# Kernel optimization log

Hardware: AMD Instinct MI355X
Metric: run time of the kernel (lower is better)

Reference implementation:

```python
import jax, jax.numpy as jnp
import numpy as np

B, S, H, NH = 2, 2048, 1024, 16
DH = H // NH
FF = 4 * H
EPS = 1e-5


def setup_inputs() -> dict:
    key = jax.random.key(0)
    ks = jax.random.split(key, 16)
    sd = 0.02
    inp = {
        "x": jax.random.normal(ks[0], (B, S, H), dtype=jnp.float32),
        "Wq": jax.random.normal(ks[1], (H, H), dtype=jnp.float32) * sd,
        "bq": jnp.zeros((H,), jnp.float32),
        "Wk": jax.random.normal(ks[2], (H, H), dtype=jnp.float32) * sd,
        "bk": jnp.zeros((H,), jnp.float32),
        "Wv": jax.random.normal(ks[3], (H, H), dtype=jnp.float32) * sd,
        "bv": jnp.zeros((H,), jnp.float32),
        "Wo": jax.random.normal(ks[4], (H, H), dtype=jnp.float32) * sd,
        "bo": jnp.zeros((H,), jnp.float32),
        "W1": jax.random.normal(ks[5], (H, FF), dtype=jnp.float32) * sd,
        "b1": jnp.zeros((FF,), jnp.float32),
        "W2": jax.random.normal(ks[6], (FF, H), dtype=jnp.float32) * sd,
        "b2": jnp.zeros((H,), jnp.float32),
        "g1": jnp.ones((H,), jnp.float32),
        "be1": jnp.zeros((H,), jnp.float32),
        "g2": jnp.ones((H,), jnp.float32),
        "be2": jnp.zeros((H,), jnp.float32),
    }
    return inp


def _layernorm(x, g, b):
    mu = jnp.mean(x, axis=-1, keepdims=True)
    var = jnp.mean(jnp.square(x - mu), axis=-1, keepdims=True)
    return (x - mu) * jax.lax.rsqrt(var + EPS) * g + b


def _block(x, Wq, bq, Wk, bk, Wv, bv, Wo, bo, W1, b1, W2, b2, g1, be1, g2, be2):
    # pre-LN attention
    h = _layernorm(x, g1, be1)
    q = (h @ Wq + bq).reshape(B, S, NH, DH)
    k = (h @ Wk + bk).reshape(B, S, NH, DH)
    v = (h @ Wv + bv).reshape(B, S, NH, DH)
    scale = DH ** -0.5
    scores = jnp.einsum("bqhd,bkhd->bhqk", q, k) * scale  # [B,NH,S,S]
    causal = jnp.tril(jnp.ones((S, S), dtype=bool))
    scores = jnp.where(causal, scores, -jnp.inf)
    attn = jax.nn.softmax(scores, axis=-1)
    out = jnp.einsum("bhqk,bkhd->bqhd", attn, v).reshape(B, S, H)
    x = x + (out @ Wo + bo)
    # pre-LN FFN with exact GELU (torch nn.GELU default)
    h = _layernorm(x, g2, be2)
    h = jax.nn.gelu(h @ W1 + b1, approximate=False)
    return x + (h @ W2 + b2)


def reference(x, Wq, bq, Wk, bk, Wv, bv, Wo, bo, W1, b1, W2, b2, g1, be1, g2, be2):
    return _block(x, Wq, bq, Wk, bk, Wv, bv, Wo, bo, W1, b1, W2, b2, g1, be1, g2, be2)
```

## Files before the change

### kernel.cpp

```cpp
#include <hip/hip_runtime.h>
#include <cstdint>
#include <cstddef>

typedef unsigned short u16;
typedef __attribute__((ext_vector_type(8))) __bf16 bf16v8;
typedef __attribute__((ext_vector_type(8))) unsigned short u16x8;
typedef __attribute__((ext_vector_type(4))) float f32x4;

constexpr int Bc = 2, Sc = 2048, Hc = 1024, NHc = 16, DHc = 64, FFc = 4096;
constexpr int Mc = Bc * Sc;

__device__ __forceinline__ u16 f2bf(float f) {
  unsigned u = __builtin_bit_cast(unsigned, f);
  return (u16)((u + 0x7FFFu + ((u >> 16) & 1u)) >> 16);
}

__device__ __forceinline__ int xcd_swz(int bid, int n) {
  const int q = n >> 3;
  return (bid & 7) * q + (bid >> 3);
}

__device__ __forceinline__ void gload_lds16(const void* g, void* l) {
  __builtin_amdgcn_global_load_lds(
      (const __attribute__((address_space(1))) unsigned*)(uintptr_t)g,
      (__attribute__((address_space(3))) unsigned*)(unsigned)(uintptr_t)l,
      16, 0, 0);
}

struct WP4 { const float* w0; const float* w1; const float* w2; const float* w3; };
__global__ __launch_bounds__(256) void wconv4_kernel(WP4 p, u16* __restrict__ Wt) {
  __shared__ float tile[64][65];
  const float* W = (blockIdx.z == 0) ? p.w0 : (blockIdx.z == 1) ? p.w1
                  : (blockIdx.z == 2) ? p.w2 : p.w3;
  u16* dst = Wt + (size_t)blockIdx.z * 1024 * 1024;
  const int n0 = blockIdx.x << 6, k0 = blockIdx.y << 6;
  const int t = threadIdx.x;
  const int col = t & 63, r0 = t >> 6;
#pragma unroll
  for (int i = 0; i < 16; ++i) {
    int r = (i << 2) + r0;
    tile[r][col] = W[(size_t)(k0 + r) * 1024 + n0 + col];
  }
  __syncthreads();
#pragma unroll
  for (int i = 0; i < 16; ++i) {
    int n = (i << 2) + r0;
    dst[(size_t)(n0 + n) * 1024 + k0 + col] = f2bf(tile[col][n]);
  }
}

__global__ __launch_bounds__(256) void wconv_kernel(const float* __restrict__ W,
                                                    u16* __restrict__ Wt, int K, int N) {
  __shared__ float tile[64][65];
  const int n0 = blockIdx.x << 6, k0 = blockIdx.y << 6;
  const int t = threadIdx.x;
  const int col = t & 63, r0 = t >> 6;
#pragma unroll
  for (int i = 0; i < 16; ++i) {
    int r = (i << 2) + r0;
    tile[r][col] = W[(size_t)(k0 + r) * N + n0 + col];
  }
  __syncthreads();
#pragma unroll
  for (int i = 0; i < 16; ++i) {
    int n = (i << 2) + r0;
    Wt[(size_t)(n0 + n) * K + k0 + col] = f2bf(tile[col][n]);
  }
}

__global__ __launch_bounds__(256) void ln_kernel(const float* __restrict__ x,
                                                 const float* __restrict__ g,
                                                 const float* __restrict__ be,
                                                 u16* __restrict__ y) {
  const int row = blockIdx.x;
  const int t = threadIdx.x;
  const float4 v = ((const float4*)(x + (size_t)row * Hc))[t];
  float s1 = v.x + v.y + v.z + v.w;
  float s2 = v.x * v.x + v.y * v.y + v.z * v.z + v.w * v.w;
#pragma unroll
  for (int o = 32; o > 0; o >>= 1) {
    s1 += __shfl_xor(s1, o);
    s2 += __shfl_xor(s2, o);
  }
  __shared__ float r1[4], r2[4];
  const int wave = t >> 6, lane = t & 63;
  if (lane == 0) { r1[wave] = s1; r2[wave] = s2; }
  __syncthreads();
  s1 = r1[0] + r1[1] + r1[2] + r1[3];
  s2 = r2[0] + r2[1] + r2[2] + r2[3];
  const float mu = s1 * (1.f / Hc);
  const float var = s2 * (1.f / Hc) - mu * mu;
  const float rs = rsqrtf(var + 1e-5f);
  const float4 gv = ((const float4*)g)[t];
  const float4 bv = ((const float4*)be)[t];
  ushort4 ov;
  ov.x = f2bf((v.x - mu) * rs * gv.x + bv.x);
  ov.y = f2bf((v.y - mu) * rs * gv.y + bv.y);
  ov.z = f2bf((v.z - mu) * rs * gv.z + bv.z);
  ov.w = f2bf((v.w - mu) * rs * gv.w + bv.w);
  ((ushort4*)(y + (size_t)row * Hc))[t] = ov;
}

template <int EPI>
__global__ __launch_bounds__(256, 2) void gemm_kernel(
    const u16* __restrict__ A, const u16* __restrict__ Bt,
    const float* __restrict__ bias, const float* __restrict__ res,
    u16* __restrict__ outb, float* __restrict__ outf, float* __restrict__ outf2,
    int N, int Kext, int lda, int ldb, int koff, int nx) {
  __shared__ __align__(16) char smraw[32768];
  u16 (*As)[128][32] = (u16(*)[128][32])smraw;
  u16 (*Bs)[128][32] = (u16(*)[128][32])(smraw + 16384);
  float (*Cs)[16][132] = (float(*)[16][132])smraw;

  const int t = threadIdx.x;
  const int wave = t >> 6, lane = t & 63;
  const int pid = xcd_swz(blockIdx.x, gridDim.x);
  const int bn = pid % nx, bm = pid / nx;
  const int kz = blockIdx.z;
  A += (size_t)kz * koff;
  Bt += (size_t)kz * koff;
  const int wm = wave >> 1, wn = wave & 1;
  const int fr = lane & 15, fk = (lane >> 4) << 3;

  f32x4 acc[4][4] = {};

  const int srow = (wave << 4) + (lane >> 2);
  const int scol = (lane & 3) << 3;
  const u16* Ag0 = A + (size_t)(bm * 128 + srow) * lda + scol;
  const u16* Ag1 = Ag0 + (size_t)64 * lda;
  const u16* Bg0 = Bt + (size_t)(bn * 128 + srow) * ldb + scol;
  const u16* Bg1 = Bg0 + (size_t)64 * ldb;

  const int nk = Kext >> 5;
  auto STAGE = [&](int buf, int k0) {
    gload_lds16(Ag0 + k0, &As[buf][wave << 4][0]);
    gload_lds16(Ag1 + k0, &As[buf][64 + (wave << 4)][0]);
    gload_lds16(Bg0 + k0, &Bs[buf][wave << 4][0]);
    gload_lds16(Bg1 + k0, &Bs[buf][64 + (wave << 4)][0]);
  };

  STAGE(0, 0);
  asm volatile("s_waitcnt vmcnt(0)" ::: "memory");
  __syncthreads();
  int cur = 0;
  for (int kt = 0; kt < nk; ++kt) {
    if (kt + 1 < nk) STAGE(cur ^ 1, (kt + 1) << 5);
    bf16v8 af[4], bfr[4];
#pragma unroll
    for (int i = 0; i < 4; ++i) af[i] = *(const bf16v8*)&As[cur][(wm << 6) + (i << 4) + fr][fk];
#pragma unroll
    for (int j = 0; j < 4; ++j) bfr[j] = *(const bf16v8*)&Bs[cur][(wn << 6) + (j << 4) + fr][fk];
    __builtin_amdgcn_s_setprio(1);
#pragma unroll
    for (int i = 0; i < 4; ++i)
#pragma unroll
      for (int j = 0; j < 4; ++j)
        acc[i][j] = __builtin_amdgcn_mfma_f32_16x16x32_bf16(af[i], bfr[j], acc[i][j], 0, 0, 0);
    __builtin_amdgcn_s_setprio(0);
    asm volatile("s_waitcnt vmcnt(0)" ::: "memory");
    __syncthreads();
    cur ^= 1;
  }

  const int cr = (lane >> 4) << 2, cc = lane & 15;
  const int b2 = t >> 7, u = t & 127, lr = u >> 3, c0 = (u & 7) << 4;
  float* fdst = (EPI == 3 && kz) ? outf2 : outf;

  for (int i = 0; i < 4; ++i) {
#pragma unroll
    for (int j = 0; j < 4; ++j) {
      int col = (wn << 6) + (j << 4) + cc;
      float bz = 0.f;
      if constexpr (EPI != 3) bz = bias[(bn << 7) + col];
#pragma unroll
      for (int r = 0; r < 4; ++r) Cs[wm][cr + r][col] = acc[i][j][r] + bz;
    }
    __syncthreads();
    {
      const float* crow = &Cs[b2][lr][c0];
      f32x4 v0 = *(const f32x4*)(crow);
      f32x4 v1 = *(const f32x4*)(crow + 4);
      f32x4 v2 = *(const f32x4*)(crow + 8);
      f32x4 v3 = *(const f32x4*)(crow + 12);
      const int grow = (bm << 7) + (b2 << 6) + (i << 4) + lr;
      const int gc = (bn << 7) + c0;
      const size_t base = (size_t)grow * N + gc;
      if constexpr (EPI == 0 || EPI == 1) {
        float vv[16];
#pragma unroll
        for (int k = 0; k < 4; ++k) { vv[k] = v0[k]; vv[4 + k] = v1[k]; vv[8 + k] = v2[k]; vv[12 + k] = v3[k]; }
        if constexpr (EPI == 1) {
#pragma unroll
          for (int k = 0; k < 16; ++k)
            vv[k] = 0.5f * vv[k] * (1.0f + erff(vv[k] * 0.70710678118654752f));
        }
        u16x8 o0, o1;
#pragma unroll
        for (int k = 0; k < 8; ++k) { o0[k] = f2bf(vv[k]); o1[k] = f2bf(vv[8 + k]); }
        *(u16x8*)&outb[base] = o0;
        *(u16x8*)&outb[base + 8] = o1;
      } else {
        if constexpr (EPI == 2) {
          const f32x4* rp = (const f32x4*)&res[base];
          v0 += rp[0]; v1 += rp[1]; v2 += rp[2]; v3 += rp[3];
        }
        f32x4* op = (f32x4*)&fdst[base];
        op[0] = v0; op[1] = v1; op[2] = v2; op[3] = v3;
      }
    }
    __syncthreads();
  }
}

template <int EPI>
__global__ __launch_bounds__(256, 2) void gemm_p_kernel(
    const u16* __restrict__ A, const u16* __restrict__ Bt,
    const float* __restrict__ bias, const float* __restrict__ res,
    u16* __restrict__ outb, float* __restrict__ outf, float* __restrict__ outf2,
    int N, int Kext, int lda, int ldb, int koff, int nx) {
  __shared__ __align__(16) char smraw[49152];
  u16 (*As)[128][32] = (u16(*)[128][32])smraw;
  u16 (*Bs)[128][32] = (u16(*)[128][32])(smraw + 24576);
  float (*Cs)[16][132] = (float(*)[16][132])smraw;

  const int t = threadIdx.x;
  const int wave = t >> 6, lane = t & 63;
  const int pid = xcd_swz(blockIdx.x, gridDim.x);
  const int bn = pid % nx, bm = pid / nx;
  const int kz = blockIdx.z;
  A += (size_t)kz * koff;
  Bt += (size_t)kz * koff;
  const int wm = wave >> 1, wn = wave & 1;
  const int fr = lane & 15, fk = (lane >> 4) << 3;

  f32x4 acc[4][4] = {};

  const int srow = (wave << 4) + (lane >> 2);
  const int scol = (lane & 3) << 3;
  const u16* Ag0 = A + (size_t)(bm * 128 + srow) * lda + scol;
  const u16* Ag1 = Ag0 + (size_t)64 * lda;
  const u16* Bg0 = Bt + (size_t)(bn * 128 + srow) * ldb + scol;
  const u16* Bg1 = Bg0 + (size_t)64 * ldb;

  const int nk = Kext >> 5;
  auto STAGE = [&](int buf, int k0) {
    gload_lds16(Ag0 + k0, &As[buf][wave << 4][0]);
    gload_lds16(Ag1 + k0, &As[buf][64 + (wave << 4)][0]);
    gload_lds16(Bg0 + k0, &Bs[buf][wave << 4][0]);
    gload_lds16(Bg1 + k0, &Bs[buf][64 + (wave << 4)][0]);
  };

  STAGE(0, 0);
  STAGE(1, 32);
  int cur = 0;
  for (int kt = 0; kt < nk; ++kt) {
    if (kt + 2 < nk) {
      int sb = cur + 2; if (sb >= 3) sb -= 3;
      STAGE(sb, (kt + 2) << 5);
      asm volatile("s_waitcnt vmcnt(8)" ::: "memory");
    } else if (kt + 1 < nk) {
      asm volatile("s_waitcnt vmcnt(4)" ::: "memory");
    } else {
      asm volatile("s_waitcnt vmcnt(0)" ::: "memory");
    }
    __builtin_amdgcn_s_barrier();
    bf16v8 af[4], bfr[4];
#pragma unroll
    for (int i = 0; i < 4; ++i) af[i] = *(const bf16v8*)&As[cur][(wm << 6) + (i << 4) + fr][fk];
#pragma unroll
    for (int j = 0; j < 4; ++j) bfr[j] = *(const bf16v8*)&Bs[cur][(wn << 6) + (j << 4) + fr][fk];
    asm volatile("s_waitcnt lgkmcnt(0)" ::: "memory");
    __builtin_amdgcn_s_barrier();
    __builtin_amdgcn_s_setprio(1);
#pragma unroll
    for (int i = 0; i < 4; ++i)
#pragma unroll
      for (int j = 0; j < 4; ++j)
        acc[i][j] = __builtin_amdgcn_mfma_f32_16x16x32_bf16(af[i], bfr[j], acc[i][j], 0, 0, 0);
    __builtin_amdgcn_s_setprio(0);
    cur = (cur + 1 == 3) ? 0 : cur + 1;
  }
  __syncthreads();

  const int cr = (lane >> 4) << 2, cc = lane & 15;
  const int b2 = t >> 7, u = t & 127, lr = u >> 3, c0 = (u & 7) << 4;
  float* fdst = (EPI == 3 && kz) ? outf2 : outf;

  for (int i = 0; i < 4; ++i) {
#pragma unroll
    for (int j = 0; j < 4; ++j) {
      int col = (wn << 6) + (j << 4) + cc;
      float bz = 0.f;
      if constexpr (EPI != 3) bz = bias[(bn << 7) + col];
#pragma unroll
      for (int r = 0; r < 4; ++r) Cs[wm][cr + r][col] = acc[i][j][r] + bz;
    }
    __syncthreads();
    {
      const float* crow = &Cs[b2][lr][c0];
      f32x4 v0 = *(const f32x4*)(crow);
      f32x4 v1 = *(const f32x4*)(crow + 4);
      f32x4 v2 = *(const f32x4*)(crow + 8);
      f32x4 v3 = *(const f32x4*)(crow + 12);
      const int grow = (bm << 7) + (b2 << 6) + (i << 4) + lr;
      const int gc = (bn << 7) + c0;
      const size_t base = (size_t)grow * N + gc;
      if constexpr (EPI == 0 || EPI == 1) {
        float vv[16];
#pragma unroll
        for (int k = 0; k < 4; ++k) { vv[k] = v0[k]; vv[4 + k] = v1[k]; vv[8 + k] = v2[k]; vv[12 + k] = v3[k]; }
        if constexpr (EPI == 1) {
#pragma unroll
          for (int k = 0; k < 16; ++k)
            vv[k] = 0.5f * vv[k] * (1.0f + erff(vv[k] * 0.70710678118654752f));
        }
        u16x8 o0, o1;
#pragma unroll
        for (int k = 0; k < 8; ++k) { o0[k] = f2bf(vv[k]); o1[k] = f2bf(vv[8 + k]); }
        *(u16x8*)&outb[base] = o0;
        *(u16x8*)&outb[base + 8] = o1;
      } else {
        if constexpr (EPI == 2) {
          const f32x4* rp = (const f32x4*)&res[base];
          v0 += rp[0]; v1 += rp[1]; v2 += rp[2]; v3 += rp[3];
        }
        f32x4* op = (f32x4*)&fdst[base];
        op[0] = v0; op[1] = v1; op[2] = v2; op[3] = v3;
      }
    }
    __syncthreads();
  }
}

__global__ __launch_bounds__(256, 2) void qkv_gemm_kernel(
    const u16* __restrict__ A, const u16* __restrict__ Bt,
    const float* __restrict__ bq, const float* __restrict__ bk,
    const float* __restrict__ bv,
    u16* __restrict__ Qb, u16* __restrict__ Kb, u16* __restrict__ Vtg) {
  constexpr int K = 1024;
  __shared__ __align__(16) char smraw[49152];
  u16 (*As)[128][32] = (u16(*)[128][32])smraw;
  u16 (*Bs)[128][32] = (u16(*)[128][32])(smraw + 24576);
  float (*Cs)[16][132] = (float(*)[16][132])smraw;

  const int t = threadIdx.x;
  const int wave = t >> 6, lane = t & 63;
  const int pid = xcd_swz(blockIdx.x, 768);
  const int bn = pid % 24, bm = pid / 24;
  const int wm = wave >> 1, wn = wave & 1;
  const int fr = lane & 15, fk = (lane >> 4) << 3;
  const int seg = bn >> 3;

  f32x4 acc[4][4] = {};

  const int srow = (wave << 4) + (lane >> 2);
  const int scol = (lane & 3) << 3;
  const u16* Ag0 = A + (size_t)(bm * 128 + srow) * K + scol;
  const u16* Ag1 = Ag0 + (size_t)64 * K;
  const u16* Bg0 = Bt + (size_t)(bn * 128 + srow) * K + scol;
  const u16* Bg1 = Bg0 + (size_t)64 * K;

  const int nk = K >> 5;
  auto STAGE = [&](int buf, int k0) {
    gload_lds16(Ag0 + k0, &As[buf][wave << 4][0]);
    gload_lds16(Ag1 + k0, &As[buf][64 + (wave << 4)][0]);
    gload_lds16(Bg0 + k0, &Bs[buf][wave << 4][0]);
    gload_lds16(Bg1 + k0, &Bs[buf][64 + (wave << 4)][0]);
  };

  STAGE(0, 0);
  STAGE(1, 32);
  int cur = 0;
  for (int kt = 0; kt < nk; ++kt) {
    if (kt + 2 < nk) {
      int sb = cur + 2; if (sb >= 3) sb -= 3;
      STAGE(sb, (kt + 2) << 5);
      asm volatile("s_waitcnt vmcnt(8)" ::: "memory");
    } else if (kt + 1 < nk) {
      asm volatile("s_waitcnt vmcnt(4)" ::: "memory");
    } else {
      asm volatile("s_waitcnt vmcnt(0)" ::: "memory");
    }
    __builtin_amdgcn_s_barrier();
    bf16v8 af[4], bfr[4];
#pragma unroll
    for (int i = 0; i < 4; ++i) af[i] = *(const bf16v8*)&As[cur][(wm << 6) + (i << 4) + fr][fk];
#pragma unroll
    for (int j = 0; j < 4; ++j) bfr[j] = *(const bf16v8*)&Bs[cur][(wn << 6) + (j << 4) + fr][fk];
    asm volatile("s_waitcnt lgkmcnt(0)" ::: "memory");
    __builtin_amdgcn_s_barrier();
    __builtin_amdgcn_s_setprio(1);
#pragma unroll
    for (int i = 0; i < 4; ++i)
#pragma unroll
      for (int j = 0; j < 4; ++j)
        acc[i][j] = __builtin_amdgcn_mfma_f32_16x16x32_bf16(af[i], bfr[j], acc[i][j], 0, 0, 0);
    __builtin_amdgcn_s_setprio(0);
    cur = (cur + 1 == 3) ? 0 : cur + 1;
  }
  __syncthreads();

  const int cr = (lane >> 4) << 2, cc = lane & 15;
  const int b2 = t >> 7, u = t & 127, lr = u >> 3, c0 = (u & 7) << 4;
  const float* bp = (seg == 0) ? bq : (seg == 1) ? bk : bv;

  for (int i = 0; i < 4; ++i) {
#pragma unroll
    for (int j = 0; j < 4; ++j) {
      int col = (wn << 6) + (j << 4) + cc;
      float bz = bp[((bn << 7) + col) & 1023];
#pragma unroll
      for (int r = 0; r < 4; ++r) Cs[wm][cr + r][col] = acc[i][j][r] + bz;
    }
    __syncthreads();
    if (seg < 2) {
      const float* crow = &Cs[b2][lr][c0];
      f32x4 v0 = *(const f32x4*)(crow);
      f32x4 v1 = *(const f32x4*)(crow + 4);
      f32x4 v2 = *(const f32x4*)(crow + 8);
      f32x4 v3 = *(const f32x4*)(crow + 12);
      const int grow = (bm << 7) + (b2 << 6) + (i << 4) + lr;
      const int cn0 = (((bn & 7) << 7) + c0);
      u16* dst = (seg == 0) ? Qb : Kb;
      u16x8 o0, o1;
#pragma unroll
      for (int k = 0; k < 4; ++k) {
        o0[k] = f2bf(v0[k]); o0[4 + k] = f2bf(v1[k]);
        o1[k] = f2bf(v2[k]); o1[4 + k] = f2bf(v3[k]);
      }
      *(u16x8*)&dst[(size_t)grow * 1024 + cn0] = o0;
      *(u16x8*)&dst[(size_t)grow * 1024 + cn0 + 8] = o1;
    } else {
      const int cv = ((bn & 7) << 7) + u;
      const int h = cv >> 6, dh = cv & 63;
#pragma unroll
      for (int oct = 0; oct < 2; ++oct) {
        u16x8 o;
#pragma unroll
        for (int k = 0; k < 8; ++k) o[k] = f2bf(Cs[b2][(oct << 3) + k][u]);
        const int srow2 = (bm << 7) + (b2 << 6) + (i << 4) + (oct << 3);
        const int bb = srow2 >> 11, s = srow2 & 2047;
        size_t idx = ((size_t)(bb * 16 + h)) * (64 * 2048) + (size_t)dh * 2048 + s;
        *(u16x8*)&Vtg[idx] = o;
      }
    }
    __syncthreads();
  }
}

__global__ __launch_bounds__(256) void combine_kernel(float* __restrict__ out,
                                                      const float* __restrict__ p0,
                                                      const float* __restrict__ p1,
                                                      const float* __restrict__ bias) {
  const int i = blockIdx.x * 256 + threadIdx.x;
  f32x4 o = ((f32x4*)out)[i];
  f32x4 a = ((const f32x4*)p0)[i];
  f32x4 b = ((const f32x4*)p1)[i];
  const int col = (i << 2) & 1023;
  f32x4 bb = *(const f32x4*)&bias[col];
  o += a + b + bb;
  ((f32x4*)out)[i] = o;
}

__global__ __launch_bounds__(256, 3) void attn_kernel(const u16* __restrict__ Q,
                                                      const u16* __restrict__ Kb,
                                                      const u16* __restrict__ Vt,
                                                      u16* __restrict__ O) {
  constexpr float CS = 0.18033688011112042f;
  constexpr float M2 = 8.0f;
  const int pid = xcd_swz(blockIdx.x, 512);
  const int bx = pid & 15, bh = pid >> 4;
  const int t = threadIdx.x, wave = t >> 6, lane = t & 63;
  const int fr = lane & 15, fk = (lane >> 4) << 3;

  __shared__ u16 Ks[2][64][72];
  __shared__ u16 Vs[2][64][72];
  __shared__ u16 Ps[4][16][72];

  const size_t base = ((size_t)(bh >> 4) * Sc) * Hc + (bh & 15) * DHc;
  const u16* Qp = Q + base;
  const u16* Kp = Kb + base;
  const u16* Vp = Vt + (size_t)bh * (64 * 2048);

  const int r_st = t >> 3;
  const int co_st = (t & 7) << 3;

  bf16v8 ones;
#pragma unroll
  for (int k = 0; k < 8; ++k) ones[k] = (__bf16)1.0f;

  for (int half = 0; half < 2; ++half) {
    const int qt = half ? (31 - bx) : bx;
    const int q0 = qt << 6;
    const int nt = qt + 1;

    const int qrow = q0 + (wave << 4) + fr;
    const bf16v8 qf0 = *(const bf16v8*)&Qp[(size_t)qrow * Hc + fk];
    const bf16v8 qf1 = *(const bf16v8*)&Qp[(size_t)qrow * Hc + 32 + fk];

    f32x4 oacc[4] = {};
    f32x4 osum = {};

    const int crow0 = q0 + (wave << 4) + ((lane >> 4) << 2);

    u16x8 rk0, rk1, rv0, rv1;
    auto LD = [&](int kv0) {
      rk0 = *(const u16x8*)&Kp[(size_t)(kv0 + r_st) * Hc + co_st];
      rk1 = *(const u16x8*)&Kp[(size_t)(kv0 + 32 + r_st) * Hc + co_st];
      rv0 = *(const u16x8*)&Vp[(size_t)r_st * 2048 + kv0 + co_st];
      rv1 = *(const u16x8*)&Vp[(size_t)(32 + r_st) * 2048 + kv0 + co_st];
    };
    auto WR = [&](int buf) {
      *(u16x8*)&Ks[buf][r_st][co_st] = rk0;
      *(u16x8*)&Ks[buf][32 + r_st][co_st] = rk1;
      *(u16x8*)&Vs[buf][r_st][co_st] = rv0;
      *(u16x8*)&Vs[buf][32 + r_st][co_st] = rv1;
    };

    LD(0);
    WR(0);
    __syncthreads();
    int cur = 0;
    for (int it = 0; it < nt; ++it) {
      const int kv0 = it << 6;
      const bool hasnext = (it + 1 < nt);
      if (hasnext) LD(kv0 + 64);

      f32x4 sc[4];
      __builtin_amdgcn_s_setprio(1);
#pragma unroll
      for (int c = 0; c < 4; ++c) {
        bf16v8 kf0 = *(const bf16v8*)&Ks[cur][(c << 4) + fr][fk];
        bf16v8 kf1 = *(const bf16v8*)&Ks[cur][(c << 4) + fr][32 + fk];
        f32x4 a = {0.f, 0.f, 0.f, 0.f};
        a = __builtin_amdgcn_mfma_f32_16x16x32_bf16(qf0, kf0, a, 0, 0, 0);
        a = __builtin_amdgcn_mfma_f32_16x16x32_bf16(qf1, kf1, a, 0, 0, 0);
        sc[c] = a;
      }
      __builtin_amdgcn_s_setprio(0);

      if (kv0 + 64 > q0) {
#pragma unroll
        for (int c = 0; c < 4; ++c)
#pragma unroll
          for (int r = 0; r < 4; ++r) {
            int kv = kv0 + (c << 4) + fr;
            if (kv > crow0 + r) sc[c][r] = -INFINITY;
          }
      }

#pragma unroll
      for (int c = 0; c < 4; ++c)
#pragma unroll
        for (int r = 0; r < 4; ++r) {
          float p = exp2f(fmaf(sc[c][r], CS, -M2));
          Ps[wave][((lane >> 4) << 2) + r][(c << 4) + fr] = f2bf(p);
        }

      const bf16v8 pa0 = *(const bf16v8*)&Ps[wave][fr][fk];
      const bf16v8 pa1 = *(const bf16v8*)&Ps[wave][fr][32 + fk];
      __builtin_amdgcn_s_setprio(1);
#pragma unroll
      for (int f = 0; f < 4; ++f) {
        bf16v8 vf0 = *(const bf16v8*)&Vs[cur][(f << 4) + fr][fk];
        bf16v8 vf1 = *(const bf16v8*)&Vs[cur][(f << 4) + fr][32 + fk];
        oacc[f] = __builtin_amdgcn_mfma_f32_16x16x32_bf16(pa0, vf0, oacc[f], 0, 0, 0);
        oacc[f] = __builtin_amdgcn_mfma_f32_16x16x32_bf16(pa1, vf1, oacc[f], 0, 0, 0);
      }
      osum = __builtin_amdgcn_mfma_f32_16x16x32_bf16(pa0, ones, osum, 0, 0, 0);
      osum = __builtin_amdgcn_mfma_f32_16x16x32_bf16(pa1, ones, osum, 0, 0, 0);
      __builtin_amdgcn_s_setprio(0);

      if (hasnext) WR(cur ^ 1);
      __syncthreads();
      cur ^= 1;
    }
#pragma unroll
    for (int r = 0; r < 4; ++r) {
      float inv = 1.0f / osum[r];
      int row = crow0 + r;
#pragma unroll
      for (int f = 0; f < 4; ++f)
        O[base + (size_t)row * Hc + (f << 4) + fr] = f2bf(oacc[f][r] * inv);
    }
    __syncthreads();
  }
}

extern "C" void kernel_launch(void* const* d_in, const int* in_sizes, int n_in,
                              void* d_out, int out_size, void* d_ws, size_t ws_size,
                              hipStream_t stream) {
  const float* x  = (const float*)d_in[0];
  const float* Wq = (const float*)d_in[1];
  const float* bq = (const float*)d_in[2];
  const float* Wk = (const float*)d_in[3];
  const float* bk = (const float*)d_in[4];
  const float* Wv = (const float*)d_in[5];
  const float* bv = (const float*)d_in[6];
  const float* Wo = (const float*)d_in[7];
  const float* bo = (const float*)d_in[8];
  const float* W1 = (const float*)d_in[9];
  const float* b1 = (const float*)d_in[10];
  const float* W2 = (const float*)d_in[11];
  const float* b2 = (const float*)d_in[12];
  const float* g1 = (const float*)d_in[13];
  const float* be1 = (const float*)d_in[14];
  const float* g2 = (const float*)d_in[15];
  const float* be2 = (const float*)d_in[16];
  float* out = (float*)d_out;

  char* ws = (char*)d_ws;
  const size_t MB = 1024 * 1024;
  u16* wqkv = (u16*)(ws + 0 * MB);
  u16* wo   = (u16*)(ws + 6 * MB);
  u16* w1   = (u16*)(ws + 8 * MB);
  u16* w2   = (u16*)(ws + 16 * MB);
  u16* lnb  = (u16*)(ws + 24 * MB);
  u16* Qb   = (u16*)(ws + 32 * MB);
  u16* Kb   = (u16*)(ws + 40 * MB);
  u16* Vtg  = (u16*)(ws + 48 * MB);
  u16* Ob   = (u16*)(ws + 56 * MB);
  u16* H1   = (u16*)(ws + 32 * MB);
  float* p0 = (float*)(ws + 64 * MB);
  float* p1 = (float*)(ws + 0 * MB);

  dim3 blk(256);
  WP4 wp{Wq, Wk, Wv, Wo};
  wconv4_kernel<<<dim3(16, 16, 4), blk, 0, stream>>>(wp, wqkv);
  wconv_kernel<<<dim3(64, 16), blk, 0, stream>>>(W1, w1, 1024, 4096);
  wconv_kernel<<<dim3(16, 64), blk, 0, stream>>>(W2, w2, 4096, 1024);

  ln_kernel<<<Mc, blk, 0, stream>>>(x, g1, be1, lnb);

  qkv_gemm_kernel<<<dim3(768), blk, 0, stream>>>(lnb, wqkv, bq, bk, bv, Qb, Kb, Vtg);

  attn_kernel<<<dim3(512), blk, 0, stream>>>(Qb, Kb, Vtg, Ob);

  gemm_p_kernel<2><<<dim3(256), blk, 0, stream>>>(Ob, wo, bo, x, nullptr, out, nullptr,
                                                  1024, 1024, 1024, 1024, 0, 8);

  ln_kernel<<<Mc, blk, 0, stream>>>(out, g2, be2, lnb);

  gemm_kernel<1><<<dim3(1024), blk, 0, stream>>>(lnb, w1, b1, nullptr, H1, nullptr, nullptr,
                                                 4096, 1024, 1024, 1024, 0, 32);

  gemm_p_kernel<3><<<dim3(256, 1, 2), blk, 0, stream>>>(H1, w2, nullptr, nullptr, nullptr, p0, p1,
                                                        1024, 2048, 4096, 4096, 2048, 8);
  combine_kernel<<<dim3(4096), blk, 0, stream>>>(out, p0, p1, b2);
}
```

Before: 247.9 us.

## Drop split-K for FFN down-projection and merge W1/W2 conversion launches

```diff
diff --git a/kernel.cpp b/kernel.cpp
--- a/kernel.cpp
+++ b/kernel.cpp
@@ -49,10 +49,16 @@
   }
 }
 
-__global__ __launch_bounds__(256) void wconv_kernel(const float* __restrict__ W,
-                                                    u16* __restrict__ Wt, int K, int N) {
+struct WP2 { const float* w1; const float* w2; };
+__global__ __launch_bounds__(256) void wconv12_kernel(WP2 p, u16* __restrict__ d1,
+                                                      u16* __restrict__ d2) {
   __shared__ float tile[64][65];
-  const int n0 = blockIdx.x << 6, k0 = blockIdx.y << 6;
+  const int z = blockIdx.z;
+  const float* W = z ? p.w2 : p.w1;
+  u16* dst = z ? d2 : d1;
+  const int K = z ? 4096 : 1024, N = z ? 1024 : 4096;
+  const int nb = N >> 6;
+  const int n0 = (blockIdx.x % nb) << 6, k0 = (blockIdx.x / nb) << 6;
   const int t = threadIdx.x;
   const int col = t & 63, r0 = t >> 6;
 #pragma unroll
@@ -64,7 +70,7 @@
 #pragma unroll
   for (int i = 0; i < 16; ++i) {
     int n = (i << 2) + r0;
-    Wt[(size_t)(n0 + n) * K + k0 + col] = f2bf(tile[col][n]);
+    dst[(size_t)(n0 + n) * K + k0 + col] = f2bf(tile[col][n]);
   }
 }
 
@@ -105,8 +111,8 @@
 __global__ __launch_bounds__(256, 2) void gemm_kernel(
     const u16* __restrict__ A, const u16* __restrict__ Bt,
     const float* __restrict__ bias, const float* __restrict__ res,
-    u16* __restrict__ outb, float* __restrict__ outf, float* __restrict__ outf2,
-    int N, int Kext, int lda, int ldb, int koff, int nx) {
+    u16* __restrict__ outb, float* __restrict__ outf,
+    int N, int Kext, int lda, int ldb, int nx) {
   __shared__ __align__(16) char smraw[32768];
   u16 (*As)[128][32] = (u16(*)[128][32])smraw;
   u16 (*Bs)[128][32] = (u16(*)[128][32])(smraw + 16384);
@@ -116,9 +122,6 @@
   const int wave = t >> 6, lane = t & 63;
   const int pid = xcd_swz(blockIdx.x, gridDim.x);
   const int bn = pid % nx, bm = pid / nx;
-  const int kz = blockIdx.z;
-  A += (size_t)kz * koff;
-  Bt += (size_t)kz * koff;
   const int wm = wave >> 1, wn = wave & 1;
   const int fr = lane & 15, fk = (lane >> 4) << 3;
 
@@ -164,14 +167,12 @@
 
   const int cr = (lane >> 4) << 2, cc = lane & 15;
   const int b2 = t >> 7, u = t & 127, lr = u >> 3, c0 = (u & 7) << 4;
-  float* fdst = (EPI == 3 && kz) ? outf2 : outf;
 
   for (int i = 0; i < 4; ++i) {
 #pragma unroll
     for (int j = 0; j < 4; ++j) {
       int col = (wn << 6) + (j << 4) + cc;
-      float bz = 0.f;
-      if constexpr (EPI != 3) bz = bias[(bn << 7) + col];
+      float bz = bias[(bn << 7) + col];
 #pragma unroll
       for (int r = 0; r < 4; ++r) Cs[wm][cr + r][col] = acc[i][j][r] + bz;
     }
@@ -200,11 +201,9 @@
         *(u16x8*)&outb[base] = o0;
         *(u16x8*)&outb[base + 8] = o1;
       } else {
-        if constexpr (EPI == 2) {
-          const f32x4* rp = (const f32x4*)&res[base];
-          v0 += rp[0]; v1 += rp[1]; v2 += rp[2]; v3 += rp[3];
-        }
-        f32x4* op = (f32x4*)&fdst[base];
+        const f32x4* rp = (const f32x4*)&res[base];
+        v0 += rp[0]; v1 += rp[1]; v2 += rp[2]; v3 += rp[3];
+        f32x4* op = (f32x4*)&outf[base];
         op[0] = v0; op[1] = v1; op[2] = v2; op[3] = v3;
       }
     }
@@ -216,8 +215,8 @@
 __global__ __launch_bounds__(256, 2) void gemm_p_kernel(
     const u16* __restrict__ A, const u16* __restrict__ Bt,
     const float* __restrict__ bias, const float* __restrict__ res,
-    u16* __restrict__ outb, float* __restrict__ outf, float* __restrict__ outf2,
-    int N, int Kext, int lda, int ldb, int koff, int nx) {
+    u16* __restrict__ outb, float* __restrict__ outf,
+    int N, int Kext, int lda, int ldb, int nx) {
   __shared__ __align__(16) char smraw[49152];
   u16 (*As)[128][32] = (u16(*)[128][32])smraw;
   u16 (*Bs)[128][32] = (u16(*)[128][32])(smraw + 24576);
@@ -227,9 +226,6 @@
   const int wave = t >> 6, lane = t & 63;
   const int pid = xcd_swz(blockIdx.x, gridDim.x);
   const int bn = pid % nx, bm = pid / nx;
-  const int kz = blockIdx.z;
-  A += (size_t)kz * koff;
-  Bt += (size_t)kz * koff;
   const int wm = wave >> 1, wn = wave & 1;
   const int fr = lane & 15, fk = (lane >> 4) << 3;
 
@@ -284,14 +280,12 @@
 
   const int cr = (lane >> 4) << 2, cc = lane & 15;
   const int b2 = t >> 7, u = t & 127, lr = u >> 3, c0 = (u & 7) << 4;
-  float* fdst = (EPI == 3 && kz) ? outf2 : outf;
 
   for (int i = 0; i < 4; ++i) {
 #pragma unroll
     for (int j = 0; j < 4; ++j) {
       int col = (wn << 6) + (j << 4) + cc;
-      float bz = 0.f;
-      if constexpr (EPI != 3) bz = bias[(bn << 7) + col];
+      float bz = bias[(bn << 7) + col];
 #pragma unroll
       for (int r = 0; r < 4; ++r) Cs[wm][cr + r][col] = acc[i][j][r] + bz;
     }
@@ -320,11 +314,9 @@
         *(u16x8*)&outb[base] = o0;
         *(u16x8*)&outb[base + 8] = o1;
       } else {
-        if constexpr (EPI == 2) {
-          const f32x4* rp = (const f32x4*)&res[base];
-          v0 += rp[0]; v1 += rp[1]; v2 += rp[2]; v3 += rp[3];
-        }
-        f32x4* op = (f32x4*)&fdst[base];
+        const f32x4* rp = (const f32x4*)&res[base];
+        v0 += rp[0]; v1 += rp[1]; v2 += rp[2]; v3 += rp[3];
+        f32x4* op = (f32x4*)&outf[base];
         op[0] = v0; op[1] = v1; op[2] = v2; op[3] = v3;
       }
     }
@@ -446,20 +438,6 @@
     }
     __syncthreads();
   }
-}
-
-__global__ __launch_bounds__(256) void combine_kernel(float* __restrict__ out,
-                                                      const float* __restrict__ p0,
-                                                      const float* __restrict__ p1,
-                                                      const float* __restrict__ bias) {
-  const int i = blockIdx.x * 256 + threadIdx.x;
-  f32x4 o = ((f32x4*)out)[i];
-  f32x4 a = ((const f32x4*)p0)[i];
-  f32x4 b = ((const f32x4*)p1)[i];
-  const int col = (i << 2) & 1023;
-  f32x4 bb = *(const f32x4*)&bias[col];
-  o += a + b + bb;
-  ((f32x4*)out)[i] = o;
 }
 
 __global__ __launch_bounds__(256, 3) void attn_kernel(const u16* __restrict__ Q,
@@ -621,14 +599,12 @@
   u16* Vtg  = (u16*)(ws + 48 * MB);
   u16* Ob   = (u16*)(ws + 56 * MB);
   u16* H1   = (u16*)(ws + 32 * MB);
-  float* p0 = (float*)(ws + 64 * MB);
-  float* p1 = (float*)(ws + 0 * MB);
 
   dim3 blk(256);
   WP4 wp{Wq, Wk, Wv, Wo};
   wconv4_kernel<<<dim3(16, 16, 4), blk, 0, stream>>>(wp, wqkv);
-  wconv_kernel<<<dim3(64, 16), blk, 0, stream>>>(W1, w1, 1024, 4096);
-  wconv_kernel<<<dim3(16, 64), blk, 0, stream>>>(W2, w2, 4096, 1024);
+  WP2 wp2{W1, W2};
+  wconv12_kernel<<<dim3(1024, 1, 2), blk, 0, stream>>>(wp2, w1, w2);
 
   ln_kernel<<<Mc, blk, 0, stream>>>(x, g1, be1, lnb);
 
@@ -636,15 +612,14 @@
 
   attn_kernel<<<dim3(512), blk, 0, stream>>>(Qb, Kb, Vtg, Ob);
 
-  gemm_p_kernel<2><<<dim3(256), blk, 0, stream>>>(Ob, wo, bo, x, nullptr, out, nullptr,
-                                                  1024, 1024, 1024, 1024, 0, 8);
+  gemm_p_kernel<2><<<dim3(256), blk, 0, stream>>>(Ob, wo, bo, x, nullptr, out,
+                                                  1024, 1024, 1024, 1024, 8);
 
   ln_kernel<<<Mc, blk, 0, stream>>>(out, g2, be2, lnb);
 
-  gemm_kernel<1><<<dim3(1024), blk, 0, stream>>>(lnb, w1, b1, nullptr, H1, nullptr, nullptr,
-                                                 4096, 1024, 1024, 1024, 0, 32);
-
-  gemm_p_kernel<3><<<dim3(256, 1, 2), blk, 0, stream>>>(H1, w2, nullptr, nullptr, nullptr, p0, p1,
-                                                        1024, 2048, 4096, 4096, 2048, 8);
-  combine_kernel<<<dim3(4096), blk, 0, stream>>>(out, p0, p1, b2);
-}
+  gemm_kernel<1><<<dim3(1024), blk, 0, stream>>>(lnb, w1, b1, nullptr, H1, nullptr,
+                                                 4096, 1024, 1024, 1024, 32);
+
+  gemm_p_kernel<2><<<dim3(256), blk, 0, stream>>>(H1, w2, b2, out, nullptr, out,
+                                                  1024, 4096, 4096, 4096, 8);
+}
```

After: 247.7 us. About the same (-0.1%).
